# Optimization experiments

Measured on AMD Instinct MI355X. Metric: run time of the kernel, lower is better.

## Reference

```python
import jax, jax.numpy as jnp
import numpy as np

T = 19          # TIME_STEPS from the source
N = 20000
EMB = 64        # embedding_dim
HID = 128       # hidden_dim
SCALE = 4.0     # InputEmbedding scale
ENC_STEPS = 8   # LRP code: encoder weights for t < 8, decoder after


def setup_inputs():
    key = jax.random.key(0)
    ks = jax.random.split(key, 16)
    obs = jax.random.normal(ks[0], (T, N, 2), dtype=jnp.float32) * 5.0
    # tracks appear at random start times -> NaN before start (drives track_mask)
    starts = jax.random.randint(ks[1], (N,), 0, 10)
    active = jnp.arange(T)[:, None] >= starts[None, :]
    obs = jnp.where(active[:, :, None], obs, jnp.nan)
    goals = jax.random.normal(ks[2], (N, 2), dtype=jnp.float32)

    def p(k, shape):
        return jax.random.normal(k, shape, dtype=jnp.float32) * 0.05

    return {
        "obs": obs, "goals": goals,
        "w_emb": p(ks[3], (EMB, 2)), "b_emb": p(ks[4], (EMB,)),
        "w_ih_e": p(ks[5], (4 * HID, EMB)), "b_ih_e": p(ks[6], (4 * HID,)),
        "w_hh_e": p(ks[7], (4 * HID, HID)), "b_hh_e": p(ks[8], (4 * HID,)),
        "w_ih_d": p(ks[9], (4 * HID, EMB)), "b_ih_d": p(ks[10], (4 * HID,)),
        "w_hh_d": p(ks[11], (4 * HID, HID)), "b_hh_d": p(ks[12], (4 * HID,)),
        "w_out": p(ks[13], (5, HID)), "b_out": p(ks[14], (5,)),
    }


def _lstm_cell(x, h, c, w_ih, b_ih, w_hh, b_hh):
    # torch.nn.LSTMCell: gate order i, f, g, o
    gates = x @ w_ih.T + b_ih + h @ w_hh.T + b_hh  # [n, 4H]
    i, f, g, o = jnp.split(gates, 4, axis=-1)
    i, f, o = jax.nn.sigmoid(i), jax.nn.sigmoid(f), jax.nn.sigmoid(o)
    g = jnp.tanh(g)
    c2 = f * c + i * g
    h2 = o * jnp.tanh(c2)
    return h2, c2


def _hidden2normal(h, w_out, b_out):
    n = h @ w_out.T + b_out  # [n, 5]
    return jnp.concatenate([
        n[:, :2],
        0.01 + 0.2 * jax.nn.sigmoid(n[:, 2:4]),  # sigmas
        0.7 * jax.nn.sigmoid(n[:, 4:5]),          # rho
    ], axis=1)


def _run_steps(obs1_seq, obs2_seq, h, c, w_emb, b_emb, w_ih, b_ih, w_hh, b_hh, w_out, b_out):
    def step(carry, ob):
        h, c = carry
        o1, o2 = ob
        # track_mask: active iff neither position is NaN (masked gather in torch)
        mask = ~(jnp.isnan(o1[:, 0]) | jnp.isnan(o2[:, 0]))
        m = mask[:, None]
        vel = jnp.where(m, o2 - o1, 0.0)                      # sanitize NaNs
        emb = jax.nn.relu((vel * SCALE) @ w_emb.T + b_emb)    # InputEmbedding
        h2, c2 = _lstm_cell(emb, h, c, w_ih, b_ih, w_hh, b_hh)
        normal = jnp.where(m, _hidden2normal(h2, w_out, b_out), 0.0)
        # scatter updated state back only for active tracks
        return (jnp.where(m, h2, h), jnp.where(m, c2, c)), normal

    (h, c), normals = jax.lax.scan(step, (h, c), (obs1_seq, obs2_seq))
    return h, c, normals


def reference(obs, goals, w_emb, b_emb, w_ih_e, b_ih_e, w_hh_e, b_hh_e,
              w_ih_d, b_ih_d, w_hh_d, b_hh_d, w_out, b_out):
    del goals  # goal_flag=False: goal embedding branch disabled
    n = obs.shape[1]
    h = jnp.zeros((n, HID), dtype=obs.dtype)
    c = jnp.zeros((n, HID), dtype=obs.dtype)
    o1, o2 = obs[:-1], obs[1:]
    h, c, n_enc = _run_steps(o1[:ENC_STEPS], o2[:ENC_STEPS], h, c,
                             w_emb, b_emb, w_ih_e, b_ih_e, w_hh_e, b_hh_e, w_out, b_out)
    h, c, n_dec = _run_steps(o1[ENC_STEPS:], o2[ENC_STEPS:], h, c,
                             w_emb, b_emb, w_ih_d, b_ih_d, w_hh_d, b_hh_d, w_out, b_out)
    return jnp.concatenate([n_enc, n_dec], axis=0)  # [T-1, N, 5]
```

## Files before the change

### kernel.cpp

```cpp
#include <hip/hip_runtime.h>

#define T_OUT 18
#define NAG   20000
#define EMBD  64
#define HIDD  128
#define APB   80
#define SH    136
#define SE    72

typedef _Float16 half8 __attribute__((ext_vector_type(8)));
typedef float    f32x4 __attribute__((ext_vector_type(4)));

__device__ __forceinline__ float rcpf(float x) { return __builtin_amdgcn_rcpf(x); }
__device__ __forceinline__ float sigmf(float x) { return rcpf(1.0f + __expf(-x)); }

__global__
__attribute__((amdgpu_flat_work_group_size(512, 512), amdgpu_waves_per_eu(2, 2)))
void lstm_seq_kernel(
    const float* __restrict__ obs,
    const float* __restrict__ w_emb,  const float* __restrict__ b_emb,
    const float* __restrict__ w_ih_e, const float* __restrict__ b_ih_e,
    const float* __restrict__ w_hh_e, const float* __restrict__ b_hh_e,
    const float* __restrict__ w_ih_d, const float* __restrict__ b_ih_d,
    const float* __restrict__ w_hh_d, const float* __restrict__ b_hh_d,
    const float* __restrict__ w_out,  const float* __restrict__ b_out,
    float* __restrict__ out)
{
  __shared__ __align__(16) _Float16 h_s[2][APB * SH];
  __shared__ __align__(16) _Float16 e_s[APB * SE];
  __shared__ float vel_s[APB * 2];
  __shared__ float mask_s[2][APB];

  const int tid = threadIdx.x;
  const int wv  = tid >> 6;
  const int ln  = tid & 63;
  const int l15 = ln & 15;
  const int lg  = ln >> 4;
  const int a0  = blockIdx.x * APB;
  const int po  = tid - 320;
  const bool obsOwner = ((unsigned)po) < APB;

  for (int i = tid; i < APB * SH; i += 512) h_s[0][i] = (_Float16)0.f;

  const float we0 = 4.f * w_emb[ln * 2 + 0];
  const float we1 = 4.f * w_emb[ln * 2 + 1];
  const float be  = b_emb[ln];

  float o2x = 0.f, o2y = 0.f;
  if (obsOwner) {
    int a = a0 + po;
    float o1x = obs[(0 * NAG + a) * 2 + 0];
    float o2x_ = obs[(1 * NAG + a) * 2 + 0], o2y_ = obs[(1 * NAG + a) * 2 + 1];
    float o1y = obs[(0 * NAG + a) * 2 + 1];
    bool ok = !__builtin_isnan(o1x) && !__builtin_isnan(o2x_);
    mask_s[0][po] = ok ? 1.f : 0.f;
    vel_s[po * 2 + 0] = ok ? (o2x_ - o1x) : 0.f;
    vel_s[po * 2 + 1] = ok ? (o2y_ - o1y) : 0.f;
    o2x = o2x_; o2y = o2y_;
  }

  half8 fih[4][2];
  half8 fhh[4][4];
  half8 fout[4];
  float bsum[4], bo;

  {
    int j = l15;
    #pragma unroll
    for (int ks = 0; ks < 4; ks++) {
      half8 v;
      #pragma unroll
      for (int q = 0; q < 8; q++) {
        float x = (j < 5) ? w_out[j * HIDD + ks * 32 + lg * 8 + q] : 0.f;
        v[q] = (_Float16)x;
      }
      fout[ks] = v;
    }
    bo = (j < 5) ? b_out[j] : 0.f;
  }

  auto load_phase = [&](const float* wih, const float* bih,
                        const float* whh, const float* bhh) {
    #pragma unroll
    for (int n = 0; n < 4; n++) {
      int row = n * 128 + wv * 16 + l15;
      #pragma unroll
      for (int ks = 0; ks < 2; ks++) {
        const float* p = wih + row * EMBD + ks * 32 + lg * 8;
        half8 v;
        #pragma unroll
        for (int q = 0; q < 8; q++) v[q] = (_Float16)p[q];
        fih[n][ks] = v;
      }
      #pragma unroll
      for (int ks = 0; ks < 4; ks++) {
        const float* p = whh + row * HIDD + ks * 32 + lg * 8;
        half8 v;
        #pragma unroll
        for (int q = 0; q < 8; q++) v[q] = (_Float16)p[q];
        fhh[n][ks] = v;
      }
      bsum[n] = bih[row] + bhh[row];
    }
  };

  auto emb_compute = [&]() {
    #pragma unroll
    for (int k = 0; k < 10; k++) {
      int a = wv + 8 * k;
      float vx = vel_s[a * 2], vy = vel_s[a * 2 + 1];
      float e = fmaf(vx, we0, fmaf(vy, we1, be));
      e_s[a * SE + ln] = (_Float16)fmaxf(e, 0.f);
    }
  };

  load_phase(w_ih_e, b_ih_e, w_hh_e, b_hh_e);
  __syncthreads();
  emb_compute();
  __syncthreads();

  float c_r[5][4];
  float h_r[5][4];
  #pragma unroll
  for (int m = 0; m < 5; m++)
    #pragma unroll
    for (int r = 0; r < 4; r++) { c_r[m][r] = 0.f; h_r[m][r] = 0.f; }

  const int hid = wv * 16 + l15;

  #pragma unroll 1
  for (int t = 0; t < T_OUT; t++) {
    if (t == 8) load_phase(w_ih_d, b_ih_d, w_hh_d, b_hh_d);

    const int idx  = t & 1;
    const int nidx = idx ^ 1;

    float n2x = 0.f, n2y = 0.f;
    if (t + 1 < T_OUT && obsOwner) {
      int a = a0 + po;
      n2x = obs[((size_t)(t + 2) * NAG + a) * 2 + 0];
      n2y = obs[((size_t)(t + 2) * NAG + a) * 2 + 1];
    }

    #pragma unroll
    for (int m = 0; m < 5; m++) {
      f32x4 acc[4];
      #pragma unroll
      for (int n = 0; n < 4; n++)
        acc[n] = f32x4{bsum[n], bsum[n], bsum[n], bsum[n]};

      #pragma unroll
      for (int ks = 0; ks < 2; ks++) {
        half8 av = *(const half8*)&e_s[(m * 16 + l15) * SE + ks * 32 + lg * 8];
        #pragma unroll
        for (int n = 0; n < 4; n++)
          acc[n] = __builtin_amdgcn_mfma_f32_16x16x32_f16(av, fih[n][ks], acc[n], 0, 0, 0);
      }
      #pragma unroll
      for (int ks = 0; ks < 4; ks++) {
        half8 av = *(const half8*)&h_s[idx][(m * 16 + l15) * SH + ks * 32 + lg * 8];
        #pragma unroll
        for (int n = 0; n < 4; n++)
          acc[n] = __builtin_amdgcn_mfma_f32_16x16x32_f16(av, fhh[n][ks], acc[n], 0, 0, 0);
      }

      float c2a[4], ova[4];
      #pragma unroll
      for (int r = 0; r < 4; r++) {
        float ai = acc[0][r], af = acc[1][r];
        float ag_ = acc[2][r], ao = acc[3][r];
        float ei = __expf(-ai), ef = __expf(-af);
        float eo = __expf(-ao), eg = __expf(-2.f * ag_);
        float di = 1.f + ei, df = 1.f + ef, dd = 1.f + eo, dg = 1.f + eg;
        float p1 = rcpf(di * df);
        float iv = df * p1, fv = di * p1;
        float p2 = rcpf(dd * dg);
        float ov = dg * p2;
        float gv = fmaf(2.f, dd * p2, -1.f);
        c2a[r] = fmaf(fv, c_r[m][r], iv * gv);
        ova[r] = ov;
      }
      float dc[4];
      #pragma unroll
      for (int r = 0; r < 4; r++) dc[r] = 1.f + __expf(-2.f * c2a[r]);
      float q01 = rcpf(dc[0] * dc[1]);
      float q23 = rcpf(dc[2] * dc[3]);
      float inv[4] = { dc[1] * q01, dc[0] * q01, dc[3] * q23, dc[2] * q23 };
      #pragma unroll
      for (int r = 0; r < 4; r++) {
        int ag = m * 16 + lg * 4 + r;
        float mk = mask_s[idx][ag];
        float th = fmaf(2.f, inv[r], -1.f);
        float h2 = ova[r] * th;
        bool on = (mk != 0.f);
        c_r[m][r] = on ? c2a[r] : c_r[m][r];
        _Float16 hh = (_Float16)(on ? h2 : h_r[m][r]);
        h_s[nidx][ag * SH + hid] = hh;
        h_r[m][r] = (float)hh;
      }
    }

    if (t + 1 < T_OUT && obsOwner) {
      float n1x = o2x, n1y = o2y;
      bool ok = !__builtin_isnan(n1x) && !__builtin_isnan(n2x);
      mask_s[nidx][po] = ok ? 1.f : 0.f;
      vel_s[po * 2 + 0] = ok ? (n2x - n1x) : 0.f;
      vel_s[po * 2 + 1] = ok ? (n2y - n1y) : 0.f;
      o2x = n2x; o2y = n2y;
    }
    __syncthreads();

    if (wv < 5) {
      f32x4 oa = f32x4{bo, bo, bo, bo};
      #pragma unroll
      for (int ks = 0; ks < 4; ks++) {
        half8 av = *(const half8*)&h_s[nidx][(wv * 16 + l15) * SH + ks * 32 + lg * 8];
        oa = __builtin_amdgcn_mfma_f32_16x16x32_f16(av, fout[ks], oa, 0, 0, 0);
      }
      int j = l15;
      #pragma unroll
      for (int r = 0; r < 4; r++) {
        int ag = wv * 16 + lg * 4 + r;
        float mk = mask_s[idx][ag];
        float nv = oa[r];
        float y;
        if (j < 2)      y = nv;
        else if (j < 4) y = 0.01f + 0.2f * sigmf(nv);
        else            y = 0.7f * sigmf(nv);
        if (j < 5) out[((size_t)t * NAG + a0 + ag) * 5 + j] = y * mk;
      }
    }
    if (t + 1 < T_OUT) emb_compute();
    __syncthreads();
  }
}

extern "C" void kernel_launch(void* const* d_in, const int* in_sizes, int n_in,
                              void* d_out, int out_size, void* d_ws, size_t ws_size,
                              hipStream_t stream) {
  const float* obs    = (const float*)d_in[0];
  const float* w_emb  = (const float*)d_in[2];
  const float* b_emb  = (const float*)d_in[3];
  const float* w_ih_e = (const float*)d_in[4];
  const float* b_ih_e = (const float*)d_in[5];
  const float* w_hh_e = (const float*)d_in[6];
  const float* b_hh_e = (const float*)d_in[7];
  const float* w_ih_d = (const float*)d_in[8];
  const float* b_ih_d = (const float*)d_in[9];
  const float* w_hh_d = (const float*)d_in[10];
  const float* b_hh_d = (const float*)d_in[11];
  const float* w_out  = (const float*)d_in[12];
  const float* b_out  = (const float*)d_in[13];
  float* out = (float*)d_out;

  lstm_seq_kernel<<<dim3(250), dim3(512), 0, stream>>>(
      obs, w_emb, b_emb, w_ih_e, b_ih_e, w_hh_e, b_hh_e,
      w_ih_d, b_ih_d, w_hh_d, b_hh_d, w_out, b_out, out);
}
```

Before: 131.6 us.

## Remove one barrier per step by deferring output head and double-buffering embeddings

```diff
diff --git a/kernel.cpp b/kernel.cpp
--- a/kernel.cpp
+++ b/kernel.cpp
@@ -5,6 +5,7 @@
 #define EMBD  64
 #define HIDD  128
 #define APB   80
+#define MT    5
 #define SH    136
 #define SE    72
 
@@ -14,8 +15,7 @@
 __device__ __forceinline__ float rcpf(float x) { return __builtin_amdgcn_rcpf(x); }
 __device__ __forceinline__ float sigmf(float x) { return rcpf(1.0f + __expf(-x)); }
 
-__global__
-__attribute__((amdgpu_flat_work_group_size(512, 512), amdgpu_waves_per_eu(2, 2)))
+__global__ __launch_bounds__(512, 2)
 void lstm_seq_kernel(
     const float* __restrict__ obs,
     const float* __restrict__ w_emb,  const float* __restrict__ b_emb,
@@ -27,9 +27,8 @@
     float* __restrict__ out)
 {
   __shared__ __align__(16) _Float16 h_s[2][APB * SH];
-  __shared__ __align__(16) _Float16 e_s[APB * SE];
-  __shared__ float vel_s[APB * 2];
-  __shared__ float mask_s[2][APB];
+  __shared__ __align__(16) _Float16 e_s[2][APB * SE];
+  __shared__ float mask_s[3][APB];
 
   const int tid = threadIdx.x;
   const int wv  = tid >> 6;
@@ -37,27 +36,13 @@
   const int l15 = ln & 15;
   const int lg  = ln >> 4;
   const int a0  = blockIdx.x * APB;
-  const int po  = tid - 320;
-  const bool obsOwner = ((unsigned)po) < APB;
+  const float2* obs2 = (const float2*)obs;
 
   for (int i = tid; i < APB * SH; i += 512) h_s[0][i] = (_Float16)0.f;
 
   const float we0 = 4.f * w_emb[ln * 2 + 0];
   const float we1 = 4.f * w_emb[ln * 2 + 1];
   const float be  = b_emb[ln];
-
-  float o2x = 0.f, o2y = 0.f;
-  if (obsOwner) {
-    int a = a0 + po;
-    float o1x = obs[(0 * NAG + a) * 2 + 0];
-    float o2x_ = obs[(1 * NAG + a) * 2 + 0], o2y_ = obs[(1 * NAG + a) * 2 + 1];
-    float o1y = obs[(0 * NAG + a) * 2 + 1];
-    bool ok = !__builtin_isnan(o1x) && !__builtin_isnan(o2x_);
-    mask_s[0][po] = ok ? 1.f : 0.f;
-    vel_s[po * 2 + 0] = ok ? (o2x_ - o1x) : 0.f;
-    vel_s[po * 2 + 1] = ok ? (o2y_ - o1y) : 0.f;
-    o2x = o2x_; o2y = o2y_;
-  }
 
   half8 fih[4][2];
   half8 fhh[4][4];
@@ -104,25 +89,36 @@
     }
   };
 
-  auto emb_compute = [&]() {
+  auto emb_mask = [&](int buf, int ts) {
+    float vx_ = 0.f, vy_ = 0.f, ok_ = 0.f;
+    if (ln < 10) {
+      int a = a0 + wv + 8 * ln;
+      float2 o1 = obs2[(size_t)ts * NAG + a];
+      float2 o2 = obs2[(size_t)(ts + 1) * NAG + a];
+      bool ok = !__builtin_isnan(o1.x) && !__builtin_isnan(o2.x);
+      vx_ = ok ? (o2.x - o1.x) : 0.f;
+      vy_ = ok ? (o2.y - o1.y) : 0.f;
+      ok_ = ok ? 1.f : 0.f;
+      mask_s[ts % 3][wv + 8 * ln] = ok_;
+    }
     #pragma unroll
     for (int k = 0; k < 10; k++) {
+      float vx = __shfl(vx_, k, 64);
+      float vy = __shfl(vy_, k, 64);
       int a = wv + 8 * k;
-      float vx = vel_s[a * 2], vy = vel_s[a * 2 + 1];
       float e = fmaf(vx, we0, fmaf(vy, we1, be));
-      e_s[a * SE + ln] = (_Float16)fmaxf(e, 0.f);
+      e_s[buf][a * SE + ln] = (_Float16)fmaxf(e, 0.f);
     }
   };
 
   load_phase(w_ih_e, b_ih_e, w_hh_e, b_hh_e);
+  emb_mask(0, 0);
   __syncthreads();
-  emb_compute();
-  __syncthreads();
-
-  float c_r[5][4];
-  float h_r[5][4];
+
+  float c_r[MT][4];
+  float h_r[MT][4];
   #pragma unroll
-  for (int m = 0; m < 5; m++)
+  for (int m = 0; m < MT; m++)
     #pragma unroll
     for (int r = 0; r < 4; r++) { c_r[m][r] = 0.f; h_r[m][r] = 0.f; }
 
@@ -134,16 +130,11 @@
 
     const int idx  = t & 1;
     const int nidx = idx ^ 1;
-
-    float n2x = 0.f, n2y = 0.f;
-    if (t + 1 < T_OUT && obsOwner) {
-      int a = a0 + po;
-      n2x = obs[((size_t)(t + 2) * NAG + a) * 2 + 0];
-      n2y = obs[((size_t)(t + 2) * NAG + a) * 2 + 1];
-    }
-
-    #pragma unroll
-    for (int m = 0; m < 5; m++) {
+    const int msC  = t % 3;
+    const int msP  = (t + 2) % 3;
+
+    #pragma unroll
+    for (int m = 0; m < MT; m++) {
       f32x4 acc[4];
       #pragma unroll
       for (int n = 0; n < 4; n++)
@@ -151,7 +142,7 @@
 
       #pragma unroll
       for (int ks = 0; ks < 2; ks++) {
-        half8 av = *(const half8*)&e_s[(m * 16 + l15) * SE + ks * 32 + lg * 8];
+        half8 av = *(const half8*)&e_s[idx][(m * 16 + l15) * SE + ks * 32 + lg * 8];
         #pragma unroll
         for (int n = 0; n < 4; n++)
           acc[n] = __builtin_amdgcn_mfma_f32_16x16x32_f16(av, fih[n][ks], acc[n], 0, 0, 0);
@@ -189,7 +180,7 @@
       #pragma unroll
       for (int r = 0; r < 4; r++) {
         int ag = m * 16 + lg * 4 + r;
-        float mk = mask_s[idx][ag];
+        float mk = mask_s[msC][ag];
         float th = fmaf(2.f, inv[r], -1.f);
         float h2 = ova[r] * th;
         bool on = (mk != 0.f);
@@ -200,38 +191,51 @@
       }
     }
 
-    if (t + 1 < T_OUT && obsOwner) {
-      float n1x = o2x, n1y = o2y;
-      bool ok = !__builtin_isnan(n1x) && !__builtin_isnan(n2x);
-      mask_s[nidx][po] = ok ? 1.f : 0.f;
-      vel_s[po * 2 + 0] = ok ? (n2x - n1x) : 0.f;
-      vel_s[po * 2 + 1] = ok ? (n2y - n1y) : 0.f;
-      o2x = n2x; o2y = n2y;
-    }
-    __syncthreads();
-
-    if (wv < 5) {
+    if (t > 0 && wv < 5) {
       f32x4 oa = f32x4{bo, bo, bo, bo};
       #pragma unroll
       for (int ks = 0; ks < 4; ks++) {
-        half8 av = *(const half8*)&h_s[nidx][(wv * 16 + l15) * SH + ks * 32 + lg * 8];
+        half8 av = *(const half8*)&h_s[idx][(wv * 16 + l15) * SH + ks * 32 + lg * 8];
         oa = __builtin_amdgcn_mfma_f32_16x16x32_f16(av, fout[ks], oa, 0, 0, 0);
       }
       int j = l15;
       #pragma unroll
       for (int r = 0; r < 4; r++) {
         int ag = wv * 16 + lg * 4 + r;
-        float mk = mask_s[idx][ag];
+        float mk = mask_s[msP][ag];
         float nv = oa[r];
         float y;
         if (j < 2)      y = nv;
         else if (j < 4) y = 0.01f + 0.2f * sigmf(nv);
         else            y = 0.7f * sigmf(nv);
-        if (j < 5) out[((size_t)t * NAG + a0 + ag) * 5 + j] = y * mk;
-      }
-    }
-    if (t + 1 < T_OUT) emb_compute();
+        if (j < 5) out[((size_t)(t - 1) * NAG + a0 + ag) * 5 + j] = y * mk;
+      }
+    }
+
+    if (t + 1 < T_OUT) emb_mask(nidx, t + 1);
+
     __syncthreads();
+  }
+
+  if (wv < 5) {
+    f32x4 oa = f32x4{bo, bo, bo, bo};
+    #pragma unroll
+    for (int ks = 0; ks < 4; ks++) {
+      half8 av = *(const half8*)&h_s[T_OUT & 1][(wv * 16 + l15) * SH + ks * 32 + lg * 8];
+      oa = __builtin_amdgcn_mfma_f32_16x16x32_f16(av, fout[ks], oa, 0, 0, 0);
+    }
+    int j = l15;
+    #pragma unroll
+    for (int r = 0; r < 4; r++) {
+      int ag = wv * 16 + lg * 4 + r;
+      float mk = mask_s[(T_OUT - 1) % 3][ag];
+      float nv = oa[r];
+      float y;
+      if (j < 2)      y = nv;
+      else if (j < 4) y = 0.01f + 0.2f * sigmf(nv);
+      else            y = 0.7f * sigmf(nv);
+      if (j < 5) out[((size_t)(T_OUT - 1) * NAG + a0 + ag) * 5 + j] = y * mk;
+    }
   }
 }
 
```

Result: slower. 139.3 us (+5.9%).

## Software-pipeline LSTM MFMA and gate math, defer output head to next step

Applied to the files above, without the earlier changes.

```diff
diff --git a/kernel.cpp b/kernel.cpp
--- a/kernel.cpp
+++ b/kernel.cpp
@@ -14,8 +14,7 @@
 __device__ __forceinline__ float rcpf(float x) { return __builtin_amdgcn_rcpf(x); }
 __device__ __forceinline__ float sigmf(float x) { return rcpf(1.0f + __expf(-x)); }
 
-__global__
-__attribute__((amdgpu_flat_work_group_size(512, 512), amdgpu_waves_per_eu(2, 2)))
+__global__ __launch_bounds__(512, 2)
 void lstm_seq_kernel(
     const float* __restrict__ obs,
     const float* __restrict__ w_emb,  const float* __restrict__ b_emb,
@@ -29,7 +28,7 @@
   __shared__ __align__(16) _Float16 h_s[2][APB * SH];
   __shared__ __align__(16) _Float16 e_s[APB * SE];
   __shared__ float vel_s[APB * 2];
-  __shared__ float mask_s[2][APB];
+  __shared__ float mask_s[3][APB];
 
   const int tid = threadIdx.x;
   const int wv  = tid >> 6;
@@ -128,12 +127,70 @@
 
   const int hid = wv * 16 + l15;
 
+#define MFMA_GROUP(ACC, M) do {                                                        \
+    _Pragma("unroll")                                                                  \
+    for (int n = 0; n < 4; n++)                                                        \
+      ACC[n] = f32x4{bsum[n], bsum[n], bsum[n], bsum[n]};                              \
+    _Pragma("unroll")                                                                  \
+    for (int ks = 0; ks < 2; ks++) {                                                   \
+      half8 av = *(const half8*)&e_s[((M) * 16 + l15) * SE + ks * 32 + lg * 8];        \
+      _Pragma("unroll")                                                                \
+      for (int n = 0; n < 4; n++)                                                      \
+        ACC[n] = __builtin_amdgcn_mfma_f32_16x16x32_f16(av, fih[n][ks], ACC[n], 0, 0, 0); \
+    }                                                                                  \
+    _Pragma("unroll")                                                                  \
+    for (int ks = 0; ks < 4; ks++) {                                                   \
+      half8 av = *(const half8*)&h_s[idx][((M) * 16 + l15) * SH + ks * 32 + lg * 8];   \
+      _Pragma("unroll")                                                                \
+      for (int n = 0; n < 4; n++)                                                      \
+        ACC[n] = __builtin_amdgcn_mfma_f32_16x16x32_f16(av, fhh[n][ks], ACC[n], 0, 0, 0); \
+    }                                                                                  \
+  } while (0)
+
+#define ELEM(ACC, M) do {                                                              \
+    float c2a[4], ova[4];                                                              \
+    _Pragma("unroll")                                                                  \
+    for (int r = 0; r < 4; r++) {                                                      \
+      float ai = ACC[0][r], af = ACC[1][r], ag_ = ACC[2][r], ao = ACC[3][r];           \
+      float ei = __expf(-ai), ef = __expf(-af);                                        \
+      float eo = __expf(-ao), eg = __expf(-2.f * ag_);                                 \
+      float di = 1.f + ei, df = 1.f + ef, dd = 1.f + eo, dg = 1.f + eg;                \
+      float p1 = rcpf(di * df);                                                        \
+      float iv = df * p1, fv = di * p1;                                                \
+      float p2 = rcpf(dd * dg);                                                        \
+      float ov = dg * p2;                                                              \
+      float gv = fmaf(2.f, dd * p2, -1.f);                                             \
+      c2a[r] = fmaf(fv, c_r[M][r], iv * gv);                                           \
+      ova[r] = ov;                                                                     \
+    }                                                                                  \
+    float dc[4];                                                                       \
+    _Pragma("unroll")                                                                  \
+    for (int r = 0; r < 4; r++) dc[r] = 1.f + __expf(-2.f * c2a[r]);                   \
+    float q01 = rcpf(dc[0] * dc[1]);                                                   \
+    float q23 = rcpf(dc[2] * dc[3]);                                                   \
+    float invv[4] = { dc[1] * q01, dc[0] * q01, dc[3] * q23, dc[2] * q23 };            \
+    _Pragma("unroll")                                                                  \
+    for (int r = 0; r < 4; r++) {                                                      \
+      int ag = (M) * 16 + lg * 4 + r;                                                  \
+      float mk = mask_s[msC][ag];                                                      \
+      float th = fmaf(2.f, invv[r], -1.f);                                             \
+      float h2 = ova[r] * th;                                                          \
+      bool on = (mk != 0.f);                                                           \
+      c_r[M][r] = on ? c2a[r] : c_r[M][r];                                             \
+      _Float16 hh = (_Float16)(on ? h2 : h_r[M][r]);                                   \
+      h_s[nidx][ag * SH + hid] = hh;                                                   \
+      h_r[M][r] = (float)hh;                                                           \
+    }                                                                                  \
+  } while (0)
+
   #pragma unroll 1
   for (int t = 0; t < T_OUT; t++) {
     if (t == 8) load_phase(w_ih_d, b_ih_d, w_hh_d, b_hh_d);
 
     const int idx  = t & 1;
     const int nidx = idx ^ 1;
+    const int msC  = t % 3;
+    const int msP  = (t + 2) % 3;
 
     float n2x = 0.f, n2y = 0.f;
     if (t + 1 < T_OUT && obsOwner) {
@@ -142,97 +199,74 @@
       n2y = obs[((size_t)(t + 2) * NAG + a) * 2 + 1];
     }
 
-    #pragma unroll
-    for (int m = 0; m < 5; m++) {
-      f32x4 acc[4];
-      #pragma unroll
-      for (int n = 0; n < 4; n++)
-        acc[n] = f32x4{bsum[n], bsum[n], bsum[n], bsum[n]};
-
-      #pragma unroll
-      for (int ks = 0; ks < 2; ks++) {
-        half8 av = *(const half8*)&e_s[(m * 16 + l15) * SE + ks * 32 + lg * 8];
-        #pragma unroll
-        for (int n = 0; n < 4; n++)
-          acc[n] = __builtin_amdgcn_mfma_f32_16x16x32_f16(av, fih[n][ks], acc[n], 0, 0, 0);
-      }
+    if (t > 0 && wv < 5) {
+      f32x4 oa = f32x4{bo, bo, bo, bo};
       #pragma unroll
       for (int ks = 0; ks < 4; ks++) {
-        half8 av = *(const half8*)&h_s[idx][(m * 16 + l15) * SH + ks * 32 + lg * 8];
-        #pragma unroll
-        for (int n = 0; n < 4; n++)
-          acc[n] = __builtin_amdgcn_mfma_f32_16x16x32_f16(av, fhh[n][ks], acc[n], 0, 0, 0);
-      }
-
-      float c2a[4], ova[4];
-      #pragma unroll
-      for (int r = 0; r < 4; r++) {
-        float ai = acc[0][r], af = acc[1][r];
-        float ag_ = acc[2][r], ao = acc[3][r];
-        float ei = __expf(-ai), ef = __expf(-af);
-        float eo = __expf(-ao), eg = __expf(-2.f * ag_);
-        float di = 1.f + ei, df = 1.f + ef, dd = 1.f + eo, dg = 1.f + eg;
-        float p1 = rcpf(di * df);
-        float iv = df * p1, fv = di * p1;
-        float p2 = rcpf(dd * dg);
-        float ov = dg * p2;
-        float gv = fmaf(2.f, dd * p2, -1.f);
-        c2a[r] = fmaf(fv, c_r[m][r], iv * gv);
-        ova[r] = ov;
-      }
-      float dc[4];
-      #pragma unroll
-      for (int r = 0; r < 4; r++) dc[r] = 1.f + __expf(-2.f * c2a[r]);
-      float q01 = rcpf(dc[0] * dc[1]);
-      float q23 = rcpf(dc[2] * dc[3]);
-      float inv[4] = { dc[1] * q01, dc[0] * q01, dc[3] * q23, dc[2] * q23 };
-      #pragma unroll
-      for (int r = 0; r < 4; r++) {
-        int ag = m * 16 + lg * 4 + r;
-        float mk = mask_s[idx][ag];
-        float th = fmaf(2.f, inv[r], -1.f);
-        float h2 = ova[r] * th;
-        bool on = (mk != 0.f);
-        c_r[m][r] = on ? c2a[r] : c_r[m][r];
-        _Float16 hh = (_Float16)(on ? h2 : h_r[m][r]);
-        h_s[nidx][ag * SH + hid] = hh;
-        h_r[m][r] = (float)hh;
-      }
-    }
-
-    if (t + 1 < T_OUT && obsOwner) {
-      float n1x = o2x, n1y = o2y;
-      bool ok = !__builtin_isnan(n1x) && !__builtin_isnan(n2x);
-      mask_s[nidx][po] = ok ? 1.f : 0.f;
-      vel_s[po * 2 + 0] = ok ? (n2x - n1x) : 0.f;
-      vel_s[po * 2 + 1] = ok ? (n2y - n1y) : 0.f;
-      o2x = n2x; o2y = n2y;
-    }
-    __syncthreads();
-
-    if (wv < 5) {
-      f32x4 oa = f32x4{bo, bo, bo, bo};
-      #pragma unroll
-      for (int ks = 0; ks < 4; ks++) {
-        half8 av = *(const half8*)&h_s[nidx][(wv * 16 + l15) * SH + ks * 32 + lg * 8];
+        half8 av = *(const half8*)&h_s[idx][(wv * 16 + l15) * SH + ks * 32 + lg * 8];
         oa = __builtin_amdgcn_mfma_f32_16x16x32_f16(av, fout[ks], oa, 0, 0, 0);
       }
       int j = l15;
       #pragma unroll
       for (int r = 0; r < 4; r++) {
         int ag = wv * 16 + lg * 4 + r;
-        float mk = mask_s[idx][ag];
+        float mk = mask_s[msP][ag];
         float nv = oa[r];
         float y;
         if (j < 2)      y = nv;
         else if (j < 4) y = 0.01f + 0.2f * sigmf(nv);
         else            y = 0.7f * sigmf(nv);
-        if (j < 5) out[((size_t)t * NAG + a0 + ag) * 5 + j] = y * mk;
-      }
-    }
+        if (j < 5) out[((size_t)(t - 1) * NAG + a0 + ag) * 5 + j] = y * mk;
+      }
+    }
+
+    {
+      f32x4 acc0[4], acc1[4];
+      MFMA_GROUP(acc0, 0);
+      MFMA_GROUP(acc1, 1);  ELEM(acc0, 0);
+      MFMA_GROUP(acc0, 2);  ELEM(acc1, 1);
+      MFMA_GROUP(acc1, 3);  ELEM(acc0, 2);
+      MFMA_GROUP(acc0, 4);  ELEM(acc1, 3);
+      ELEM(acc0, 4);
+    }
+
+    if (t + 1 < T_OUT && obsOwner) {
+      float n1x = o2x, n1y = o2y;
+      bool ok = !__builtin_isnan(n1x) && !__builtin_isnan(n2x);
+      mask_s[(t + 1) % 3][po] = ok ? 1.f : 0.f;
+      vel_s[po * 2 + 0] = ok ? (n2x - n1x) : 0.f;
+      vel_s[po * 2 + 1] = ok ? (n2y - n1y) : 0.f;
+      o2x = n2x; o2y = n2y;
+    }
+    __syncthreads();
+
     if (t + 1 < T_OUT) emb_compute();
     __syncthreads();
   }
+
+  if (wv < 5) {
+    f32x4 oa = f32x4{bo, bo, bo, bo};
+    #pragma unroll
+    for (int ks = 0; ks < 4; ks++) {
+      half8 av = *(const half8*)&h_s[T_OUT & 1][(wv * 16 + l15) * SH + ks * 32 + lg * 8];
+      oa = __builtin_amdgcn_mfma_f32_16x16x32_f16(av, fout[ks], oa, 0, 0, 0);
+    }
+    int j = l15;
+    #pragma unroll
+    for (int r = 0; r < 4; r++) {
+      int ag = wv * 16 + lg * 4 + r;
+      float mk = mask_s[(T_OUT - 1) % 3][ag];
+      float nv = oa[r];
+      float y;
+      if (j < 2)      y = nv;
+      else if (j < 4) y = 0.01f + 0.2f * sigmf(nv);
+      else            y = 0.7f * sigmf(nv);
+      if (j < 5) out[((size_t)(T_OUT - 1) * NAG + a0 + ag) * 5 + j] = y * mk;
+    }
+  }
+
+#undef MFMA_GROUP
+#undef ELEM
 }
 
 extern "C" void kernel_launch(void* const* d_in, const int* in_sizes, int n_in,
```

Result: slower. 144.2 us (+9.6%).
